# Optimization experiments

Hardware: AMD Instinct MI355X
Metric: run time of the kernel (lower is better)

Reference implementation:

```python
import jax, jax.numpy as jnp
import numpy as np

D_MODEL = 768
H = 6
DQK = 128
DV = 256
SCALE_BASE = 512.0


def _xpos(x, sign):
    """xPos rotary: x (B,T,H,d); sign=+1 for queries, -1 for keys."""
    B, T, Hn, d = x.shape
    half = d // 2
    pos = jnp.arange(T, dtype=jnp.float32)
    inv_freq = 1.0 / (10000.0 ** (jnp.arange(half, dtype=jnp.float32) / half))
    angles = pos[:, None] * inv_freq[None, :]                    # (T, half)
    zeta = (jnp.arange(half, dtype=jnp.float32) + half) / d      # (half,)
    decay = zeta[None, :] ** (sign * pos[:, None] / SCALE_BASE)  # (T, half)
    cos_a = (jnp.cos(angles) * decay)[None, :, None, :]
    sin_a = (jnp.sin(angles) * decay)[None, :, None, :]
    x1, x2 = x[..., :half], x[..., half:]
    return jnp.concatenate([x1 * cos_a - x2 * sin_a,
                            x1 * sin_a + x2 * cos_a], axis=-1)


def _decay_mask(T):
    """(H,T,T) causal decay mask, row-normalized by sqrt(row_sum)."""
    gammas = jnp.array([1.0 - 2.0 ** (-(5 + h)) for h in range(H)], dtype=jnp.float32)
    i = jnp.arange(T, dtype=jnp.float32)
    diff = i[:, None] - i[None, :]
    causal = (diff >= 0).astype(jnp.float32)
    D = (gammas[:, None, None] ** jnp.clip(diff, 0.0)[None]) * causal[None]
    row = jnp.clip(jnp.sum(D, axis=-1, keepdims=True), 1e-6)
    return D / jnp.sqrt(row)


def setup_inputs() -> dict:
    key = jax.random.key(0)
    ks = jax.random.split(key, 6)
    B, T = 2, 2048

    def xavier(k, shape):
        lim = float(np.sqrt(6.0 / (shape[0] + shape[1])))
        return jax.random.uniform(k, shape, jnp.float32, -lim, lim)

    return {
        "x": jax.random.normal(ks[0], (B, T, D_MODEL), jnp.float32),
        "Wq": xavier(ks[1], (D_MODEL, H * DQK)),
        "Wk": xavier(ks[2], (D_MODEL, H * DQK)),
        "Wv": xavier(ks[3], (D_MODEL, H * DV)),
        "Wg": xavier(ks[4], (D_MODEL, H * DV)),
        "Wo": xavier(ks[5], (H * DV, D_MODEL)),
        "gn_weight": jnp.ones((H * DV,), jnp.float32),
        "gn_bias": jnp.zeros((H * DV,), jnp.float32),
    }


def reference(x, Wq, Wk, Wv, Wg, Wo, gn_weight, gn_bias):
    B, T, _ = x.shape
    Q = (x @ Wq).reshape(B, T, H, DQK)
    K = (x @ Wk).reshape(B, T, H, DQK)
    V = (x @ Wv).reshape(B, T, H, DV)
    Q = _xpos(Q, 1.0)
    K = _xpos(K, -1.0)
    # retention scores: QK^T * scale * per-head decay mask (no softmax)
    scores = jnp.einsum('bihd,bjhd->bhij', Q, K) * (DQK ** -0.5)
    scores = scores * _decay_mask(T)[None]
    out = jnp.einsum('bhij,bjhv->bihv', scores, V)   # (B,T,H,DV)
    concat = out.reshape(B, T, H * DV)
    # GroupNorm over (channels-in-group, time) per (batch, group), as torch GN on (B,C,T)
    g = concat.transpose(0, 2, 1).reshape(B, H, DV, T)
    mean = jnp.mean(g, axis=(2, 3), keepdims=True)
    var = jnp.var(g, axis=(2, 3), keepdims=True)
    g = (g - mean) / jnp.sqrt(var + 1e-5)
    g = g.reshape(B, H * DV, T) * gn_weight[None, :, None] + gn_bias[None, :, None]
    normed = g.transpose(0, 2, 1)                    # (B,T,H*DV)
    gate = jax.nn.silu(x @ Wg)
    return (normed * gate) @ Wo
```

## Files before the change

### kernel.cpp

```cpp
#include <hip/hip_runtime.h>

typedef unsigned short u16;
typedef unsigned int u32;
typedef __attribute__((ext_vector_type(8))) short short8;
typedef __attribute__((ext_vector_type(4))) float f32x4;

#define DEV static __device__ __forceinline__

DEV float bf2f(u16 u){ u32 i = ((u32)u)<<16; float f; __builtin_memcpy(&f,&i,4); return f; }
DEV u16 f2bf(float f){ u32 i; __builtin_memcpy(&i,&f,4); u32 r = i + 0x7FFFu + ((i>>16)&1u); return (u16)(r>>16); }

DEV void gld16(const void* gp, void* lp){
  __builtin_amdgcn_global_load_lds((const __attribute__((address_space(1))) void*)gp,
                                   (__attribute__((address_space(3))) void*)lp, 16, 0, 0);
}

DEV void phase_barrier(){
  asm volatile("" ::: "memory");
  __builtin_amdgcn_sched_barrier(0);
  __builtin_amdgcn_s_barrier();
  __builtin_amdgcn_sched_barrier(0);
  asm volatile("" ::: "memory");
}

__global__ void k_prep(const float* __restrict__ x,
                       const float* __restrict__ Wq, const float* __restrict__ Wk,
                       const float* __restrict__ Wv, const float* __restrict__ Wg,
                       const float* __restrict__ Wo,
                       u16* __restrict__ xb, u16* __restrict__ WT, u16* __restrict__ WoT,
                       float4* __restrict__ tab){
  __shared__ float tile[32][33];
  int i = blockIdx.x, tid = threadIdx.x;
  if (i < 3072){
    size_t base = ((size_t)i*256 + tid)*4;
    float4 v = *(const float4*)(x + base);
    ushort4 o; o.x=f2bf(v.x); o.y=f2bf(v.y); o.z=f2bf(v.z); o.w=f2bf(v.w);
    *(ushort4*)(xb + base) = o;
  } else if (i < 7680){
    int j = i - 3072;
    const float* src; u16* dst; int N, K, bx, by;
    if (j < 576)       { src=Wq; dst=WT;             N=768;  K=768;  bx=j%24; by=j/24; }
    else if (j < 1152) { int q=j-576;  src=Wk; dst=WT+768ull*768;  N=768;  K=768;  bx=q%24; by=q/24; }
    else if (j < 2304) { int q=j-1152; src=Wv; dst=WT+1536ull*768; N=1536; K=768;  bx=q%48; by=q/48; }
    else if (j < 3456) { int q=j-2304; src=Wg; dst=WT+3072ull*768; N=1536; K=768;  bx=q%48; by=q/48; }
    else               { int q=j-3456; src=Wo; dst=WoT;            N=768;  K=1536; bx=q%24; by=q/24; }
    int n0 = bx*32, k0 = by*32;
    int tx = tid&31, ty = tid>>5;
    #pragma unroll
    for (int q=0;q<4;++q)
      tile[ty + q*8][tx] = src[(size_t)(k0 + ty + q*8)*N + n0 + tx];
    __syncthreads();
    #pragma unroll
    for (int q=0;q<4;++q)
      dst[(size_t)(n0 + ty + q*8)*K + k0 + tx] = f2bf(tile[tx][ty + q*8]);
  } else {
    int idx = (i-7680)*256 + tid;
    int t = idx>>6, j = idx&63;
    float inv_freq = expf(-(float)j * (9.210340371976184f/64.f));
    float angle = (float)t * inv_freq;
    float zeta = (float)(j + 64) * (1.f/128.f);
    float decq = exp2f(log2f(zeta) * ((float)t*(1.f/512.f)));
    float deck = 1.f/decq;
    float sn, cs; sincosf(angle, &sn, &cs);
    float4 o; o.x = cs*decq; o.y = sn*decq; o.z = cs*deck; o.w = sn*deck;
    tab[idx] = o;
  }
}

__global__ void k_xpos2(u16* __restrict__ Qr, u16* __restrict__ Kr, const float4* __restrict__ tab){
  int idx = blockIdx.x*256 + threadIdx.x;
  int jg = idx & 15;
  int h  = (idx>>4) % 6;
  int m  = (idx>>4) / 6;
  int t  = m & 2047;
  size_t base = (size_t)m*768 + h*128 + jg*4;
  ushort4 q1 = *(const ushort4*)(Qr + base);
  ushort4 q2 = *(const ushort4*)(Qr + base + 64);
  ushort4 k1 = *(const ushort4*)(Kr + base);
  ushort4 k2 = *(const ushort4*)(Kr + base + 64);
  ushort4 oq1, oq2, ok1, ok2;
  const float4* tb = tab + t*64 + jg*4;
  #pragma unroll
  for (int jj=0;jj<4;++jj){
    float4 f = tb[jj];
    float a, b2;
    a = bf2f(((const u16*)&q1)[jj]); b2 = bf2f(((const u16*)&q2)[jj]);
    ((u16*)&oq1)[jj] = f2bf(a*f.x - b2*f.y);
    ((u16*)&oq2)[jj] = f2bf(a*f.y + b2*f.x);
    a = bf2f(((const u16*)&k1)[jj]); b2 = bf2f(((const u16*)&k2)[jj]);
    ((u16*)&ok1)[jj] = f2bf(a*f.z - b2*f.w);
    ((u16*)&ok2)[jj] = f2bf(a*f.w + b2*f.z);
  }
  *(ushort4*)(Qr + base)      = oq1;
  *(ushort4*)(Qr + base + 64) = oq2;
  *(ushort4*)(Kr + base)      = ok1;
  *(ushort4*)(Kr + base + 64) = ok2;
}

__global__ void k_trans(const u16* __restrict__ Vraw, u16* __restrict__ VbTs,
                        const u16* __restrict__ Kr, u16* __restrict__ KbT){
  __shared__ u16 tile[32][33];
  int i = blockIdx.x, tid = threadIdx.x;
  int tx = tid&31, ty = tid>>5;
  if (i < 6144){
    int bh = i>>9, r = i&511;
    int t0 = (r&63)*32, v0 = (r>>6)*32;
    int b = bh/6, h = bh%6;
    float lg2g = log2f(1.f - exp2f(-(float)(5+h)));
    float dec = exp2f(lg2g * (float)(63 - ((t0 + tx) & 63)));
    #pragma unroll
    for (int q=0;q<4;++q)
      tile[ty+q*8][tx] = Vraw[(size_t)(b*2048 + t0 + ty + q*8)*1536 + h*256 + v0 + tx];
    __syncthreads();
    #pragma unroll
    for (int q=0;q<4;++q)
      VbTs[(size_t)(bh*256 + v0 + ty + q*8)*2048 + t0 + tx] = f2bf(bf2f(tile[tx][ty+q*8]) * dec);
  } else {
    int j = i - 6144;
    int bh = j>>8, r = j&255;
    int t0 = (r&63)*32, d0 = (r>>6)*32;
    int b = bh/6, h = bh%6;
    #pragma unroll
    for (int q=0;q<4;++q)
      tile[ty+q*8][tx] = Kr[(size_t)(b*2048 + t0 + ty + q*8)*768 + h*128 + d0 + tx];
    __syncthreads();
    #pragma unroll
    for (int q=0;q<4;++q)
      KbT[(size_t)(bh*128 + d0 + ty + q*8)*2048 + t0 + tx] = tile[tx][ty+q*8];
  }
}

template<int MODE, int BM>
__global__ __launch_bounds__(256)
void k_gemm(const u16* __restrict__ A, const u16* __restrict__ BT,
            int K, int N,
            u16* __restrict__ Qr, u16* __restrict__ Kr,
            u16* __restrict__ Vraw, u16* __restrict__ Gb,
            float* __restrict__ Out)
{
  constexpr int MR = BM/32;
  constexpr int ABUF = BM*128;
  __shared__ u16 As[2*BM*64];
  __shared__ u16 Bs[2*128*64];
  const int tid = threadIdx.x;
  const int w = tid>>6, l = tid&63, g = l>>4, ln = l&15;
  const int wr = w>>1, wc = w&1;
  const int m0 = blockIdx.x*BM, n0 = blockIdx.y*128;
  const f32x4 fz = {0.f,0.f,0.f,0.f};
  f32x4 acc[MR][4];
  #pragma unroll
  for (int m=0;m<MR;++m)
    #pragma unroll
    for (int n=0;n<4;++n) acc[m][n] = fz;

  auto stageA = [&](int d, int kt){
    const int k0 = kt<<6;
    #pragma unroll
    for (int i=0;i<BM/32;++i){
      int off = i*4096 + tid*16;
      int row = off>>7;
      int colb = (off&127) ^ ((row&7)<<4);
      gld16(A + (size_t)(m0+row)*K + k0 + (colb>>1), (char*)As + d*ABUF + i*4096 + w*1024);
    }
  };
  auto stageB = [&](int d, int kt){
    const int k0 = kt<<6;
    #pragma unroll
    for (int i=0;i<4;++i){
      int off = i*4096 + tid*16;
      int row = off>>7;
      int colb = (off&127) ^ ((row&7)<<4);
      gld16(BT + (size_t)(n0+row)*K + k0 + (colb>>1), (char*)Bs + d*16384 + i*4096 + w*1024);
    }
  };

  const int nt = K>>6;
  stageA(0, 0);
  stageB(0, 0);

  for (int t=0; t<nt; ++t){
    const int c = t&1, o = c^1;
    if (t+1 < nt){
      stageA(o, t+1);
      if constexpr (BM==128) asm volatile("s_waitcnt vmcnt(4)");
      else                   asm volatile("s_waitcnt vmcnt(2)");
    } else {
      asm volatile("s_waitcnt vmcnt(0)");
    }
    phase_barrier();

    const char* Ab = (const char*)As + c*ABUF;
    const char* Bb = (const char*)Bs + c*16384;
    short8 bfr[4][2];
    #pragma unroll
    for (int n=0;n<4;++n){
      int row = wc*64 + n*16 + ln;
      int sw = (row&7)<<4;
      bfr[n][0] = *(const short8*)(Bb + row*128 + ((g*16)^sw));
      bfr[n][1] = *(const short8*)(Bb + row*128 + ((64 + g*16)^sw));
    }
    #pragma unroll
    for (int m=0;m<MR/2;++m){
      int row = wr*(BM/2) + m*16 + ln;
      int sw = (row&7)<<4;
      short8 a0 = *(const short8*)(Ab + row*128 + ((g*16)^sw));
      short8 a1 = *(const short8*)(Ab + row*128 + ((64 + g*16)^sw));
      #pragma unroll
      for (int n=0;n<4;++n){
        acc[m][n] = __builtin_amdgcn_mfma_f32_16x16x32_bf16(a0, bfr[n][0], acc[m][n], 0,0,0);
        acc[m][n] = __builtin_amdgcn_mfma_f32_16x16x32_bf16(a1, bfr[n][1], acc[m][n], 0,0,0);
      }
    }
    if (t+1 < nt) stageB(o, t+1);
    #pragma unroll
    for (int m=MR/2;m<MR;++m){
      int row = wr*(BM/2) + m*16 + ln;
      int sw = (row&7)<<4;
      short8 a0 = *(const short8*)(Ab + row*128 + ((g*16)^sw));
      short8 a1 = *(const short8*)(Ab + row*128 + ((64 + g*16)^sw));
      #pragma unroll
      for (int n=0;n<4;++n){
        acc[m][n] = __builtin_amdgcn_mfma_f32_16x16x32_bf16(a0, bfr[n][0], acc[m][n], 0,0,0);
        acc[m][n] = __builtin_amdgcn_mfma_f32_16x16x32_bf16(a1, bfr[n][1], acc[m][n], 0,0,0);
      }
    }
    phase_barrier();
  }

  const int region = n0/768;
  #pragma unroll
  for (int m=0;m<MR;++m){
    int grow0 = m0 + wr*(BM/2) + m*16 + g*4;
    #pragma unroll
    for (int n=0;n<4;++n){
      int cc = n0 + wc*64 + n*16 + ln;
      #pragma unroll
      for (int r=0;r<4;++r){
        float v = acc[m][n][r];
        size_t grow = (size_t)(grow0 + r);
        if (MODE == 1){
          Out[grow*(size_t)N + cc] = v;
        } else {
          if (region==0)      Qr[grow*768 + cc] = f2bf(v);
          else if (region==1) Kr[grow*768 + (cc-768)] = f2bf(v);
          else if (region<4)  Vraw[grow*1536 + (cc-1536)] = f2bf(v);
          else { float sg = v/(1.f+__expf(-v)); Gb[grow*1536 + (cc-3072)] = f2bf(sg); }
        }
      }
    }
  }
}

__global__ __launch_bounds__(256)
void k_passA(const u16* __restrict__ VbTs, const u16* __restrict__ KbT, u16* __restrict__ Zb)
{
  __shared__ u16 Kt[128*64];
  __shared__ u16 Vt[256*64];
  const int tid = threadIdx.x, w = tid>>6, l = tid&63, g = l>>4, ln = l&15;
  const int c = blockIdx.x, bh = blockIdx.y;
  const f32x4 fz = {0.f,0.f,0.f,0.f};

  #pragma unroll
  for (int i=0;i<4;++i){
    int off = i*4096 + tid*16;
    int row = off>>7;
    int colb = (off&127) ^ ((row&7)<<4);
    gld16(KbT + (size_t)(bh*128 + row)*2048 + c*64 + (colb>>1), (char*)Kt + i*4096 + w*1024);
  }
  #pragma unroll
  for (int i=0;i<8;++i){
    int off = i*4096 + tid*16;
    int row = off>>7;
    int colb = (off&127) ^ ((row&7)<<4);
    gld16(VbTs + (size_t)(bh*256 + row)*2048 + c*64 + (colb>>1), (char*)Vt + i*4096 + w*1024);
  }
  __syncthreads();

  f32x4 acc[4][8];
  #pragma unroll
  for (int m=0;m<4;++m)
    #pragma unroll
    for (int n=0;n<8;++n) acc[m][n] = fz;

  #pragma unroll
  for (int kk=0;kk<2;++kk){
    short8 va[4], kb[8];
    #pragma unroll
    for (int m=0;m<4;++m){
      int vrow = w*64 + m*16 + ln;
      int byte = vrow*128 + ((kk*64 + g*16) ^ ((vrow&7)<<4));
      va[m] = *(const short8*)((const char*)Vt + byte);
    }
    #pragma unroll
    for (int n=0;n<8;++n){
      int krow = n*16 + ln;
      int byte = krow*128 + ((kk*64 + g*16) ^ ((krow&7)<<4));
      kb[n] = *(const short8*)((const char*)Kt + byte);
    }
    #pragma unroll
    for (int m=0;m<4;++m)
      #pragma unroll
      for (int n=0;n<8;++n)
        acc[m][n] = __builtin_amdgcn_mfma_f32_16x16x32_bf16(va[m], kb[n], acc[m][n], 0,0,0);
  }

  u16* z = Zb + (size_t)(c*12 + bh)*32768;
  #pragma unroll
  for (int m=0;m<4;++m)
    #pragma unroll
    for (int n=0;n<8;++n)
      #pragma unroll
      for (int r=0;r<4;++r){
        int v = w*64 + m*16 + g*4 + r;
        int d = n*16 + ln;
        z[v*128 + d] = f2bf(acc[m][n][r]);
      }
}

__global__ __launch_bounds__(256)
void k_scan(const u16* __restrict__ Zb, u16* __restrict__ States)
{
  int gid = blockIdx.x*256 + threadIdx.x;
  int bh = gid >> 13;
  int e0 = (gid & 8191) * 4;
  const int h = bh % 6;
  const float lg2g = log2f(1.f - exp2f(-(float)(5+h)));
  const float gl = exp2f(lg2g * 64.f);
  ushort4 z[31];
  #pragma unroll
  for (int c=0;c<31;++c)
    z[c] = *(const ushort4*)(Zb + (size_t)(c*12 + bh)*32768 + e0);
  {
    ushort4 o; o.x=0;o.y=0;o.z=0;o.w=0;
    *(ushort4*)(States + (size_t)bh*32768 + e0) = o;
  }
  float S0=0.f,S1=0.f,S2=0.f,S3=0.f;
  #pragma unroll
  for (int c=1;c<32;++c){
    ushort4 zz = z[c-1];
    S0 = gl*S0 + bf2f(zz.x); S1 = gl*S1 + bf2f(zz.y);
    S2 = gl*S2 + bf2f(zz.z); S3 = gl*S3 + bf2f(zz.w);
    ushort4 o; o.x=f2bf(S0); o.y=f2bf(S1); o.z=f2bf(S2); o.w=f2bf(S3);
    *(ushort4*)(States + (size_t)(c*12 + bh)*32768 + e0) = o;
  }
}

__global__ __launch_bounds__(256)
void k_passC(const u16* __restrict__ Qb, const u16* __restrict__ Kb,
             const u16* __restrict__ VbTs, const u16* __restrict__ States,
             float* __restrict__ Of, float* __restrict__ partials)
{
  __shared__ u16 Ks[64*128];
  __shared__ u16 Vt[256*64];
  __shared__ float Ps[64*64];
  __shared__ float red[8];
  const int tid = threadIdx.x, w = tid>>6, l = tid&63, g = l>>4, ln = l&15;
  const int c = blockIdx.x, bh = blockIdx.y, b = bh/6, h = bh%6;
  const float omg = exp2f(-(float)(5+h));
  const float gamma = 1.f - omg;
  const float lg2g = log2f(gamma);
  const float scale = 0.08838834764831845f;
  const int q0 = c*64;
  const f32x4 fz = {0.f,0.f,0.f,0.f};

  short8 aq[4];
  {
    const size_t qrow = (size_t)(b*2048 + q0 + w*16 + ln)*768 + h*128;
    #pragma unroll
    for (int kk=0;kk<4;++kk) aq[kk] = *(const short8*)(Qb + qrow + kk*32 + g*8);
  }

  #pragma unroll
  for (int i=0;i<4;++i){
    int off = i*4096 + tid*16;
    int row = off>>8;
    int colb = (off&255) ^ ((row&7)<<4);
    gld16(Kb + (size_t)(b*2048 + q0 + row)*768 + h*128 + (colb>>1),
          (char*)Ks + i*4096 + w*1024);
  }
  #pragma unroll
  for (int i=0;i<8;++i){
    int off = i*4096 + tid*16;
    int row = off>>7;
    int colb = (off&127) ^ ((row&7)<<4);
    gld16(VbTs + (size_t)(bh*256 + row)*2048 + q0 + (colb>>1),
          (char*)Vt + i*4096 + w*1024);
  }
  __syncthreads();

  f32x4 sacc[4]; sacc[0]=fz; sacc[1]=fz; sacc[2]=fz; sacc[3]=fz;
  #pragma unroll
  for (int kk=0;kk<4;++kk){
    #pragma unroll
    for (int n=0;n<4;++n){
      int row = n*16 + ln;
      int byte = row*256 + ((kk*64 + g*16) ^ ((row&7)<<4));
      short8 bk = *(const short8*)((const char*)Ks + byte);
      sacc[n] = __builtin_amdgcn_mfma_f32_16x16x32_bf16(aq[kk], bk, sacc[n], 0,0,0);
    }
  }
  #pragma unroll
  for (int n=0;n<4;++n){
    int kj = n*16 + ln;
    #pragma unroll
    for (int r=0;r<4;++r){
      int a = w*16 + g*4 + r;
      float p = (a >= kj) ? sacc[n][r] : 0.f;
      int prow = w*16 + g*4 + r;
      int byte = prow*256 + ((((n*16+ln)*4)) ^ ((prow&7)<<4));
      *(float*)((char*)Ps + byte) = p;
    }
  }
  f32x4 acc[16];
  #pragma unroll
  for (int i=0;i<16;++i) acc[i] = fz;
  #pragma unroll
  for (int kk2=0;kk2<2;++kk2){
    int prow = w*16 + ln;
    int base = prow*256;
    int c0 = kk2*128 + g*32;
    int sw = (prow&7)<<4;
    f32x4 p0 = *(const f32x4*)((const char*)Ps + base + ((c0   )^sw));
    f32x4 p1 = *(const f32x4*)((const char*)Ps + base + ((c0+16)^sw));
    short8 ap;
    #pragma unroll
    for (int jj=0;jj<4;++jj){ ap[jj] = (short)f2bf(p0[jj]); ap[4+jj] = (short)f2bf(p1[jj]); }
    #pragma unroll
    for (int n2=0;n2<16;++n2){
      int vrow = n2*16 + ln;
      int byte = vrow*128 + ((kk2*64 + g*16) ^ ((vrow&7)<<4));
      short8 bv = *(const short8*)((const char*)Vt + byte);
      acc[n2] = __builtin_amdgcn_mfma_f32_16x16x32_bf16(ap, bv, acc[n2], 0,0,0);
    }
  }
  const float gi64 = exp2f(-64.f*lg2g);
  #pragma unroll
  for (int i=0;i<16;++i){ acc[i][0]*=gi64; acc[i][1]*=gi64; acc[i][2]*=gi64; acc[i][3]*=gi64; }
  const u16* st = States + (size_t)(c*12 + bh)*32768;
  #pragma unroll
  for (int kk=0;kk<4;++kk){
    #pragma unroll
    for (int n2=0;n2<16;++n2){
      short8 sb = *(const short8*)(st + (n2*16 + ln)*128 + kk*32 + g*8);
      acc[n2] = __builtin_amdgcn_mfma_f32_16x16x32_bf16(aq[kk], sb, acc[n2], 0,0,0);
    }
  }
  float rf[4];
  #pragma unroll
  for (int r=0;r<4;++r){
    int a = w*16 + g*4 + r;
    int qi = q0 + a;
    float rs = (1.f - exp2f(lg2g*(float)(qi+1))) / omg;
    rf[r] = scale * exp2f(lg2g*(float)(a+1)) * rsqrtf(fmaxf(rs, 1e-6f));
  }
  float lsum=0.f, lsq=0.f;
  #pragma unroll
  for (int n2=0;n2<16;++n2){
    #pragma unroll
    for (int r=0;r<4;++r){
      float v = acc[n2][r]*rf[r];
      Of[(size_t)(b*2048 + q0 + w*16 + g*4 + r)*1536 + h*256 + n2*16 + ln] = v;
      lsum += v; lsq += v*v;
    }
  }
  #pragma unroll
  for (int o=32;o;o>>=1){ lsum += __shfl_xor(lsum,o,64); lsq += __shfl_xor(lsq,o,64); }
  if (l==0){ red[w*2]=lsum; red[w*2+1]=lsq; }
  __syncthreads();
  if (tid==0){
    partials[(c*12+bh)*2]   = red[0]+red[2]+red[4]+red[6];
    partials[(c*12+bh)*2+1] = red[1]+red[3]+red[5]+red[7];
  }
}

__global__ __launch_bounds__(64)
void k_redstats(const float* __restrict__ partials, float* __restrict__ stats){
  int bh = blockIdx.x, l = threadIdx.x;
  float s=0.f, q=0.f;
  if (l < 32){ s = partials[(l*12+bh)*2]; q = partials[(l*12+bh)*2+1]; }
  #pragma unroll
  for (int o=16;o;o>>=1){ s += __shfl_xor(s,o,64); q += __shfl_xor(q,o,64); }
  if (l==0){ stats[bh*2] = s; stats[bh*2+1] = q; }
}

__global__ void k_gatenorm(const float* __restrict__ Of, const u16* __restrict__ Gb,
                           const float* __restrict__ gnw, const float* __restrict__ gnb,
                           const float* __restrict__ stats, u16* __restrict__ Yb){
  size_t base = ((size_t)blockIdx.x*256 + threadIdx.x)*8;
  int m = (int)(base/1536);
  int c = (int)(base%1536);
  int bh = (m>>11)*6 + (c>>8);
  const float Ninv = 1.f/524288.f;
  float mean = stats[bh*2]*Ninv;
  float var = stats[bh*2+1]*Ninv - mean*mean;
  float rstd = rsqrtf(var + 1e-5f);
  #pragma unroll
  for (int jj=0;jj<8;++jj){
    float o = Of[base+jj];
    float nv = (o-mean)*rstd*gnw[c+jj] + gnb[c+jj];
    Yb[base+jj] = f2bf(nv * bf2f(Gb[base+jj]));
  }
}

extern "C" void kernel_launch(void* const* d_in, const int* in_sizes, int n_in,
                              void* d_out, int out_size, void* d_ws, size_t ws_size,
                              hipStream_t stream)
{
  const float* x   = (const float*)d_in[0];
  const float* Wq  = (const float*)d_in[1];
  const float* Wk  = (const float*)d_in[2];
  const float* Wv  = (const float*)d_in[3];
  const float* Wg  = (const float*)d_in[4];
  const float* Wo  = (const float*)d_in[5];
  const float* gnw = (const float*)d_in[6];
  const float* gnb = (const float*)d_in[7];
  float* out = (float*)d_out;

  char* ws = (char*)d_ws;
  u16*   xb     = (u16*)  (ws + 0);
  u16*   WT     = (u16*)  (ws + 6291456);
  u16*   Vraw   = (u16*)  (ws + 13369344);
  u16*   KbT    = (u16*)  (ws + 6291456);
  u16*   States = (u16*)  (ws + 0);
  u16*   Yb     = (u16*)  (ws + 0);
  u16*   Kr     = (u16*)  (ws + 25952256);
  u16*   Qr     = (u16*)  (ws + 32243712);
  u16*   Gb     = (u16*)  (ws + 38535168);
  u16*   WoT    = (u16*)  (ws + 51118080);
  u16*   VbTs   = (u16*)  (ws + 53477376);
  u16*   Zb     = (u16*)  (ws + 66060288);
  float* Of     = (float*)(ws + 66060288);
  float* partials = (float*)(ws + 91226112);
  float* stats  = (float*)(ws + 91230208);
  float4* tab   = (float4*)(ws + 95158272);

  k_prep<<<8192, 256, 0, stream>>>(x, Wq, Wk, Wv, Wg, Wo, xb, WT, WoT, tab);
  k_gemm<0,128><<<dim3(32,36), 256, 0, stream>>>(xb, WT, 768, 4608, Qr, Kr, Vraw, Gb, (float*)nullptr);
  k_xpos2<<<1536, 256, 0, stream>>>(Qr, Kr, tab);
  k_trans<<<9216, 256, 0, stream>>>(Vraw, VbTs, Kr, KbT);
  k_passA<<<dim3(31,12), 256, 0, stream>>>(VbTs, KbT, Zb);
  k_scan<<<384, 256, 0, stream>>>(Zb, States);
  k_passC<<<dim3(32,12), 256, 0, stream>>>(Qr, Kr, VbTs, States, Of, partials);
  k_redstats<<<12, 64, 0, stream>>>(partials, stats);
  k_gatenorm<<<3072, 256, 0, stream>>>(Of, Gb, gnw, gnb, stats, Yb);
  k_gemm<1,64><<<dim3(64,6), 256, 0, stream>>>(Yb, WoT, 1536, 768,
                                            (u16*)nullptr,(u16*)nullptr,(u16*)nullptr,(u16*)nullptr, out);
}
```

Measured before the change: 170.6 us.

## Fuse xPos into GEMM epilogue, single-buffer GEMM, bf16 intermediate output

The xPos rotary step now runs inside the QKV projection epilogue: each tile is staged through shared memory so the paired half-dimension is available, which removes the separate k_xpos2 kernel and its read/write pass over Q and K. The GEMM main loop drops its double-buffered, hand-scheduled pipeline for a simpler single-buffer loop with two __syncthreads per k-step. This loses load/compute overlap but halves shared memory use. The retention output is stored as bf16 instead of fp32, and the gate-norm kernel reads and writes with vector accesses, at a small cost in precision before normalization.

```diff
diff --git a/kernel.cpp b/kernel.cpp
--- a/kernel.cpp
+++ b/kernel.cpp
@@ -13,14 +13,6 @@
 DEV void gld16(const void* gp, void* lp){
   __builtin_amdgcn_global_load_lds((const __attribute__((address_space(1))) void*)gp,
                                    (__attribute__((address_space(3))) void*)lp, 16, 0, 0);
-}
-
-DEV void phase_barrier(){
-  asm volatile("" ::: "memory");
-  __builtin_amdgcn_sched_barrier(0);
-  __builtin_amdgcn_s_barrier();
-  __builtin_amdgcn_sched_barrier(0);
-  asm volatile("" ::: "memory");
 }
 
 __global__ void k_prep(const float* __restrict__ x,
@@ -67,36 +59,6 @@
   }
 }
 
-__global__ void k_xpos2(u16* __restrict__ Qr, u16* __restrict__ Kr, const float4* __restrict__ tab){
-  int idx = blockIdx.x*256 + threadIdx.x;
-  int jg = idx & 15;
-  int h  = (idx>>4) % 6;
-  int m  = (idx>>4) / 6;
-  int t  = m & 2047;
-  size_t base = (size_t)m*768 + h*128 + jg*4;
-  ushort4 q1 = *(const ushort4*)(Qr + base);
-  ushort4 q2 = *(const ushort4*)(Qr + base + 64);
-  ushort4 k1 = *(const ushort4*)(Kr + base);
-  ushort4 k2 = *(const ushort4*)(Kr + base + 64);
-  ushort4 oq1, oq2, ok1, ok2;
-  const float4* tb = tab + t*64 + jg*4;
-  #pragma unroll
-  for (int jj=0;jj<4;++jj){
-    float4 f = tb[jj];
-    float a, b2;
-    a = bf2f(((const u16*)&q1)[jj]); b2 = bf2f(((const u16*)&q2)[jj]);
-    ((u16*)&oq1)[jj] = f2bf(a*f.x - b2*f.y);
-    ((u16*)&oq2)[jj] = f2bf(a*f.y + b2*f.x);
-    a = bf2f(((const u16*)&k1)[jj]); b2 = bf2f(((const u16*)&k2)[jj]);
-    ((u16*)&ok1)[jj] = f2bf(a*f.z - b2*f.w);
-    ((u16*)&ok2)[jj] = f2bf(a*f.w + b2*f.z);
-  }
-  *(ushort4*)(Qr + base)      = oq1;
-  *(ushort4*)(Qr + base + 64) = oq2;
-  *(ushort4*)(Kr + base)      = ok1;
-  *(ushort4*)(Kr + base + 64) = ok2;
-}
-
 __global__ void k_trans(const u16* __restrict__ Vraw, u16* __restrict__ VbTs,
                         const u16* __restrict__ Kr, u16* __restrict__ KbT){
   __shared__ u16 tile[32][33];
@@ -136,12 +98,10 @@
             int K, int N,
             u16* __restrict__ Qr, u16* __restrict__ Kr,
             u16* __restrict__ Vraw, u16* __restrict__ Gb,
-            float* __restrict__ Out)
+            float* __restrict__ Out, const float4* __restrict__ tab)
 {
   constexpr int MR = BM/32;
-  constexpr int ABUF = BM*128;
-  __shared__ u16 As[2*BM*64];
-  __shared__ u16 Bs[2*128*64];
+  __shared__ u16 smem[BM*64 + 128*64];
   const int tid = threadIdx.x;
   const int w = tid>>6, l = tid&63, g = l>>4, ln = l&15;
   const int wr = w>>1, wc = w&1;
@@ -153,98 +113,103 @@
     #pragma unroll
     for (int n=0;n<4;++n) acc[m][n] = fz;
 
-  auto stageA = [&](int d, int kt){
+  const int nk = K>>6;
+  for (int kt=0; kt<nk; ++kt){
     const int k0 = kt<<6;
     #pragma unroll
     for (int i=0;i<BM/32;++i){
       int off = i*4096 + tid*16;
       int row = off>>7;
       int colb = (off&127) ^ ((row&7)<<4);
-      gld16(A + (size_t)(m0+row)*K + k0 + (colb>>1), (char*)As + d*ABUF + i*4096 + w*1024);
-    }
-  };
-  auto stageB = [&](int d, int kt){
-    const int k0 = kt<<6;
+      gld16(A  + (size_t)(m0+row)*K + k0 + (colb>>1), (char*)smem + i*4096 + w*1024);
+    }
     #pragma unroll
     for (int i=0;i<4;++i){
       int off = i*4096 + tid*16;
       int row = off>>7;
       int colb = (off&127) ^ ((row&7)<<4);
-      gld16(BT + (size_t)(n0+row)*K + k0 + (colb>>1), (char*)Bs + d*16384 + i*4096 + w*1024);
-    }
-  };
-
-  const int nt = K>>6;
-  stageA(0, 0);
-  stageB(0, 0);
-
-  for (int t=0; t<nt; ++t){
-    const int c = t&1, o = c^1;
-    if (t+1 < nt){
-      stageA(o, t+1);
-      if constexpr (BM==128) asm volatile("s_waitcnt vmcnt(4)");
-      else                   asm volatile("s_waitcnt vmcnt(2)");
-    } else {
-      asm volatile("s_waitcnt vmcnt(0)");
-    }
-    phase_barrier();
-
-    const char* Ab = (const char*)As + c*ABUF;
-    const char* Bb = (const char*)Bs + c*16384;
-    short8 bfr[4][2];
-    #pragma unroll
-    for (int n=0;n<4;++n){
-      int row = wc*64 + n*16 + ln;
-      int sw = (row&7)<<4;
-      bfr[n][0] = *(const short8*)(Bb + row*128 + ((g*16)^sw));
-      bfr[n][1] = *(const short8*)(Bb + row*128 + ((64 + g*16)^sw));
-    }
-    #pragma unroll
-    for (int m=0;m<MR/2;++m){
-      int row = wr*(BM/2) + m*16 + ln;
-      int sw = (row&7)<<4;
-      short8 a0 = *(const short8*)(Ab + row*128 + ((g*16)^sw));
-      short8 a1 = *(const short8*)(Ab + row*128 + ((64 + g*16)^sw));
+      gld16(BT + (size_t)(n0+row)*K + k0 + (colb>>1), (char*)smem + BM*128 + i*4096 + w*1024);
+    }
+    __syncthreads();
+    #pragma unroll
+    for (int kk=0;kk<2;++kk){
+      short8 a[MR], b[4];
+      #pragma unroll
+      for (int m=0;m<MR;++m){
+        int row = wr*(BM/2) + m*16 + ln;
+        int byte = row*128 + ((kk*64 + g*16) ^ ((row&7)<<4));
+        a[m] = *(const short8*)((const char*)smem + byte);
+      }
       #pragma unroll
       for (int n=0;n<4;++n){
-        acc[m][n] = __builtin_amdgcn_mfma_f32_16x16x32_bf16(a0, bfr[n][0], acc[m][n], 0,0,0);
-        acc[m][n] = __builtin_amdgcn_mfma_f32_16x16x32_bf16(a1, bfr[n][1], acc[m][n], 0,0,0);
+        int row = wc*64 + n*16 + ln;
+        int byte = BM*128 + row*128 + ((kk*64 + g*16) ^ ((row&7)<<4));
+        b[n] = *(const short8*)((const char*)smem + byte);
       }
-    }
-    if (t+1 < nt) stageB(o, t+1);
-    #pragma unroll
-    for (int m=MR/2;m<MR;++m){
-      int row = wr*(BM/2) + m*16 + ln;
-      int sw = (row&7)<<4;
-      short8 a0 = *(const short8*)(Ab + row*128 + ((g*16)^sw));
-      short8 a1 = *(const short8*)(Ab + row*128 + ((64 + g*16)^sw));
+      #pragma unroll
+      for (int m=0;m<MR;++m)
+        #pragma unroll
+        for (int n=0;n<4;++n)
+          acc[m][n] = __builtin_amdgcn_mfma_f32_16x16x32_bf16(a[m], b[n], acc[m][n], 0,0,0);
+    }
+    __syncthreads();
+  }
+
+  const int region = n0/768;
+  if (MODE==0 && region<2){
+    #pragma unroll
+    for (int m=0;m<MR;++m){
       #pragma unroll
       for (int n=0;n<4;++n){
-        acc[m][n] = __builtin_amdgcn_mfma_f32_16x16x32_bf16(a0, bfr[n][0], acc[m][n], 0,0,0);
-        acc[m][n] = __builtin_amdgcn_mfma_f32_16x16x32_bf16(a1, bfr[n][1], acc[m][n], 0,0,0);
+        int d = wc*64 + n*16 + ln;
+        #pragma unroll
+        for (int r=0;r<4;++r){
+          int row = wr*(BM/2) + m*16 + g*4 + r;
+          smem[row*128 + (d ^ ((row&7)<<3))] = f2bf(acc[m][n][r]);
+        }
       }
     }
-    phase_barrier();
-  }
-
-  const int region = n0/768;
-  #pragma unroll
-  for (int m=0;m<MR;++m){
-    int grow0 = m0 + wr*(BM/2) + m*16 + g*4;
-    #pragma unroll
-    for (int n=0;n<4;++n){
-      int cc = n0 + wc*64 + n*16 + ln;
-      #pragma unroll
-      for (int r=0;r<4;++r){
-        float v = acc[m][n][r];
-        size_t grow = (size_t)(grow0 + r);
-        if (MODE == 1){
-          Out[grow*(size_t)N + cc] = v;
-        } else {
-          if (region==0)      Qr[grow*768 + cc] = f2bf(v);
-          else if (region==1) Kr[grow*768 + (cc-768)] = f2bf(v);
-          else if (region<4)  Vraw[grow*1536 + (cc-1536)] = f2bf(v);
-          else { float sg = v/(1.f+__expf(-v)); Gb[grow*1536 + (cc-3072)] = f2bf(sg); }
+    __syncthreads();
+    const int hloc = (n0 - region*768) >> 7;
+    #pragma unroll
+    for (int m=0;m<MR;++m){
+      #pragma unroll
+      for (int n=0;n<4;++n){
+        int d = wc*64 + n*16 + ln;
+        int j = d & 63;
+        #pragma unroll
+        for (int r=0;r<4;++r){
+          int row = wr*(BM/2) + m*16 + g*4 + r;
+          int sw = (row&7)<<3;
+          float self = bf2f(smem[row*128 + (d ^ sw)]);
+          float part = bf2f(smem[row*128 + ((d^64) ^ sw)]);
+          size_t grow = (size_t)(m0 + row);
+          float4 f = tab[(grow & 2047)*64 + j];
+          float cs = (region==0) ? f.x : f.z;
+          float sn = (region==0) ? f.y : f.w;
+          float val = (d < 64) ? (self*cs - part*sn) : (part*sn + self*cs);
+          if (region==0) Qr[grow*768 + hloc*128 + d] = f2bf(val);
+          else           Kr[grow*768 + hloc*128 + d] = f2bf(val);
+        }
+      }
+    }
+  } else {
+    #pragma unroll
+    for (int m=0;m<MR;++m){
+      int grow0 = m0 + wr*(BM/2) + m*16 + g*4;
+      #pragma unroll
+      for (int n=0;n<4;++n){
+        int c = n0 + wc*64 + n*16 + ln;
+        #pragma unroll
+        for (int r=0;r<4;++r){
+          float v = acc[m][n][r];
+          size_t grow = (size_t)(grow0 + r);
+          if (MODE == 1){
+            Out[grow*(size_t)N + c] = v;
+          } else {
+            if (region<4) Vraw[grow*1536 + (c-1536)] = f2bf(v);
+            else { float sg = v/(1.f+__expf(-v)); Gb[grow*1536 + (c-3072)] = f2bf(sg); }
+          }
         }
       }
     }
@@ -348,7 +313,7 @@
 __global__ __launch_bounds__(256)
 void k_passC(const u16* __restrict__ Qb, const u16* __restrict__ Kb,
              const u16* __restrict__ VbTs, const u16* __restrict__ States,
-             float* __restrict__ Of, float* __restrict__ partials)
+             u16* __restrict__ Ofb, float* __restrict__ partials)
 {
   __shared__ u16 Ks[64*128];
   __shared__ u16 Vt[256*64];
@@ -459,7 +424,7 @@
     #pragma unroll
     for (int r=0;r<4;++r){
       float v = acc[n2][r]*rf[r];
-      Of[(size_t)(b*2048 + q0 + w*16 + g*4 + r)*1536 + h*256 + n2*16 + ln] = v;
+      Ofb[(size_t)(b*2048 + q0 + w*16 + g*4 + r)*1536 + h*256 + n2*16 + ln] = f2bf(v);
       lsum += v; lsq += v*v;
     }
   }
@@ -483,7 +448,7 @@
   if (l==0){ stats[bh*2] = s; stats[bh*2+1] = q; }
 }
 
-__global__ void k_gatenorm(const float* __restrict__ Of, const u16* __restrict__ Gb,
+__global__ void k_gatenorm(const u16* __restrict__ Ofb, const u16* __restrict__ Gb,
                            const float* __restrict__ gnw, const float* __restrict__ gnb,
                            const float* __restrict__ stats, u16* __restrict__ Yb){
   size_t base = ((size_t)blockIdx.x*256 + threadIdx.x)*8;
@@ -494,12 +459,16 @@
   float mean = stats[bh*2]*Ninv;
   float var = stats[bh*2+1]*Ninv - mean*mean;
   float rstd = rsqrtf(var + 1e-5f);
+  short8 ov = *(const short8*)(Ofb + base);
+  short8 gv = *(const short8*)(Gb + base);
+  short8 yo;
   #pragma unroll
   for (int jj=0;jj<8;++jj){
-    float o = Of[base+jj];
+    float o = bf2f((u16)ov[jj]);
     float nv = (o-mean)*rstd*gnw[c+jj] + gnb[c+jj];
-    Yb[base+jj] = f2bf(nv * bf2f(Gb[base+jj]));
-  }
+    yo[jj] = (short)f2bf(nv * bf2f((u16)gv[jj]));
+  }
+  *(short8*)(Yb + base) = yo;
 }
 
 extern "C" void kernel_launch(void* const* d_in, const int* in_sizes, int n_in,
@@ -529,20 +498,21 @@
   u16*   WoT    = (u16*)  (ws + 51118080);
   u16*   VbTs   = (u16*)  (ws + 53477376);
   u16*   Zb     = (u16*)  (ws + 66060288);
-  float* Of     = (float*)(ws + 66060288);
+  u16*   Ofb    = (u16*)  (ws + 66060288);
   float* partials = (float*)(ws + 91226112);
   float* stats  = (float*)(ws + 91230208);
   float4* tab   = (float4*)(ws + 95158272);
 
   k_prep<<<8192, 256, 0, stream>>>(x, Wq, Wk, Wv, Wg, Wo, xb, WT, WoT, tab);
-  k_gemm<0,128><<<dim3(32,36), 256, 0, stream>>>(xb, WT, 768, 4608, Qr, Kr, Vraw, Gb, (float*)nullptr);
-  k_xpos2<<<1536, 256, 0, stream>>>(Qr, Kr, tab);
+  k_gemm<0,128><<<dim3(32,36), 256, 0, stream>>>(xb, WT, 768, 4608, Qr, Kr, Vraw, Gb,
+                                                 (float*)nullptr, tab);
   k_trans<<<9216, 256, 0, stream>>>(Vraw, VbTs, Kr, KbT);
   k_passA<<<dim3(31,12), 256, 0, stream>>>(VbTs, KbT, Zb);
   k_scan<<<384, 256, 0, stream>>>(Zb, States);
-  k_passC<<<dim3(32,12), 256, 0, stream>>>(Qr, Kr, VbTs, States, Of, partials);
+  k_passC<<<dim3(32,12), 256, 0, stream>>>(Qr, Kr, VbTs, States, Ofb, partials);
   k_redstats<<<12, 64, 0, stream>>>(partials, stats);
-  k_gatenorm<<<3072, 256, 0, stream>>>(Of, Gb, gnw, gnb, stats, Yb);
+  k_gatenorm<<<3072, 256, 0, stream>>>(Ofb, Gb, gnw, gnb, stats, Yb);
   k_gemm<1,64><<<dim3(64,6), 256, 0, stream>>>(Yb, WoT, 1536, 768,
-                                            (u16*)nullptr,(u16*)nullptr,(u16*)nullptr,(u16*)nullptr, out);
-}
+                                            (u16*)nullptr,(u16*)nullptr,(u16*)nullptr,(u16*)nullptr,
+                                            out, (float4*)nullptr);
+}
```

Result: faster. 158.4 us (-7.1%).
